# Kernel optimization log

Hardware: AMD Instinct MI355X
Metric: run time of the kernel (lower is better)

## Reference

```python
import jax, jax.numpy as jnp
import numpy as np

V, E, F, L, S, B, C = 30522, 768, 3072, 4, 512, 32, 2


def _layernorm(x, g, b, eps=1e-5):
    mu = jnp.mean(x, axis=-1, keepdims=True)
    var = jnp.var(x, axis=-1, keepdims=True)
    return (x - mu) * jax.lax.rsqrt(var + eps) * g + b


def setup_inputs() -> dict:
    key = jax.random.key(0)
    ks = jax.random.split(key, 24)
    s = 0.02
    inp = {
        "input_ids": jax.random.randint(ks[0], (S, B), 0, V),
        "tok_emb": jax.random.normal(ks[1], (V, E), jnp.float32) * s,
        "pos_emb": jax.random.normal(ks[2], (512, E), jnp.float32) * s,
        "Wq": jax.random.normal(ks[3], (L, E, E), jnp.float32) * s,
        "bq": jnp.zeros((L, E), jnp.float32),
        "Wk": jax.random.normal(ks[4], (L, E, E), jnp.float32) * s,
        "bk": jnp.zeros((L, E), jnp.float32),
        "Wv": jax.random.normal(ks[5], (L, E, E), jnp.float32) * s,
        "bv": jnp.zeros((L, E), jnp.float32),
        "Wo": jax.random.normal(ks[6], (L, E, E), jnp.float32) * s,
        "bo": jnp.zeros((L, E), jnp.float32),
        "g1": jnp.ones((L, E), jnp.float32),
        "beta1": jnp.zeros((L, E), jnp.float32),
        "g2": jnp.ones((L, E), jnp.float32),
        "beta2": jnp.zeros((L, E), jnp.float32),
        "W1": jax.random.normal(ks[7], (L, E, F), jnp.float32) * s,
        "bf1": jnp.zeros((L, F), jnp.float32),
        "W2": jax.random.normal(ks[8], (L, F, E), jnp.float32) * s,
        "bf2": jnp.zeros((L, E), jnp.float32),
        "Wc": jax.random.normal(ks[9], (E, C), jnp.float32) * s,
        "bc": jnp.zeros((C,), jnp.float32),
    }
    return inp


def reference(input_ids, tok_emb, pos_emb, Wq, bq, Wk, bk, Wv, bv, Wo, bo,
              g1, beta1, g2, beta2, W1, bf1, W2, bf2, Wc, bc):
    s_len = input_ids.shape[0]
    # x: [S, B, E] (seq-first, as in the original)
    x = tok_emb[input_ids] + pos_emb[jnp.arange(s_len)][:, None, :]
    scale = 1.0 / jnp.sqrt(jnp.asarray(E, x.dtype))
    for l in range(L):
        Q = x @ Wq[l] + bq[l]
        K = x @ Wk[l] + bk[l]
        Vv = x @ Wv[l] + bv[l]
        # NOTE: faithful to source bug: attention mixes over BATCH dim, scores [S,B,B]
        scores = jnp.einsum('sbe,sce->sbc', Q, K) * scale
        attn = jax.nn.softmax(scores, axis=-1)
        ao = jnp.einsum('sbc,sce->sbe', attn, Vv)
        ao = ao @ Wo[l] + bo[l]
        x = _layernorm(x + ao, g1[l], beta1[l])
        h = jax.nn.relu(x @ W1[l] + bf1[l]) @ W2[l] + bf2[l]
        x = _layernorm(x + h, g2[l], beta2[l])
    cls = x[0]                      # [B, E]
    return cls @ Wc + bc            # [B, C]
```

## Files before the change

### kernel.cpp

```cpp
#include <hip/hip_runtime.h>


#define E_DIM 768
#define F_DIM 3072
#define L_NUM 4
#define S_LEN 512
#define NTOK  (S_LEN * 32)
#define QKVN  (3 * E_DIM)

typedef float f32x4 __attribute__((ext_vector_type(4)));
typedef unsigned int u32x4 __attribute__((ext_vector_type(4)));
typedef unsigned short u16x4 __attribute__((ext_vector_type(4)));

__device__ __forceinline__ float bf2f(unsigned int bits) {
    return __uint_as_float(bits << 16);
}
__device__ __forceinline__ unsigned short f2bf(float f) {
    unsigned int x = __float_as_uint(f);
    return (unsigned short)((x + 0x7fffu + ((x >> 16) & 1u)) >> 16);
}

#define GLD16(gp, lp) \
    __builtin_amdgcn_global_load_lds( \
        (const __attribute__((address_space(1))) unsigned int*)(gp), \
        (__attribute__((address_space(3))) unsigned int*)(lp), 16, 0, 0)

__global__ __launch_bounds__(256)
void tr_k(const float* __restrict__ src, unsigned short* __restrict__ dst,
          int R, int C, size_t ss, size_t ds)
{
    __shared__ float tile[32][33];
    src += (size_t)blockIdx.z * ss;
    dst += (size_t)blockIdx.z * ds;
    const int r0 = blockIdx.y * 32, c0 = blockIdx.x * 32;
    const int tr = threadIdx.x >> 3, tc = (threadIdx.x & 7) * 4;
    f32x4 v = *(const f32x4*)(src + (size_t)(r0 + tr) * C + c0 + tc);
    tile[tr][tc + 0] = v[0]; tile[tr][tc + 1] = v[1];
    tile[tr][tc + 2] = v[2]; tile[tr][tc + 3] = v[3];
    __syncthreads();
    u16x4 o;
    o[0] = f2bf(tile[tc + 0][tr]); o[1] = f2bf(tile[tc + 1][tr]);
    o[2] = f2bf(tile[tc + 2][tr]); o[3] = f2bf(tile[tc + 3][tr]);
    *(u16x4*)(dst + (size_t)(c0 + tr) * R + r0 + tc) = o;
}

__global__ __launch_bounds__(256)
void biascat_k(const float* __restrict__ bq, const float* __restrict__ bk,
               const float* __restrict__ bv, float* __restrict__ bqkv)
{
    const int i = blockIdx.x * 256 + threadIdx.x;
    if (i >= L_NUM * QKVN) return;
    const int l = i / QKVN, n = i % QKVN;
    float v;
    if (n < 768)       v = bq[l * 768 + n];
    else if (n < 1536) v = bk[l * 768 + n - 768];
    else               v = bv[l * 768 + n - 1536];
    bqkv[i] = v;
}

__global__ __launch_bounds__(256)
void embed_k(const int* __restrict__ ids, const float* __restrict__ tok,
             const float* __restrict__ pos, float* __restrict__ xf,
             unsigned short* __restrict__ xb)
{
    const int row = blockIdx.x;
    const int s = row >> 5;
    const int id = ids[row];
    const size_t rb = (size_t)row * E_DIM;
    for (int e = threadIdx.x; e < E_DIM; e += 256) {
        float v = tok[(size_t)id * E_DIM + e] + pos[(size_t)s * E_DIM + e];
        xf[rb + e] = v;
        xb[rb + e] = f2bf(v);
    }
}

template<int MODE>
__global__ __launch_bounds__(256)
void gemm2_k(const unsigned short* __restrict__ A, const unsigned short* __restrict__ BT,
             const float* __restrict__ bias, void* __restrict__ Cout,
             int lda, int ldb, int ldc, int K, int JT)
{
    __shared__ unsigned short As[128 * 64];
    __shared__ unsigned short Bs[128 * 64];
    const int t = threadIdx.x;
    const int d = blockIdx.x;
    const int qd = d >> 3, rd = d & 7;
    const int jb = qd % JT;
    const int ib = rd + 8 * (qd / JT);
    const int i0 = ib * 128, j0 = jb * 128;

    const int lane = t & 63, wave = t >> 6;
    const int wm = wave >> 1, wn = wave & 1;
    const int lr = lane & 15, lg = lane >> 4;

    const int sr = t >> 3;
    const int sc = (t & 7) * 8;

    f32x4 acc[4][4];
    #pragma unroll
    for (int mf = 0; mf < 4; mf++)
        #pragma unroll
        for (int nf = 0; nf < 4; nf++) acc[mf][nf] = (f32x4)0.0f;

    const unsigned short* Ab = A  + (size_t)(i0 + sr) * lda + sc;
    const unsigned short* Bb = BT + (size_t)(j0 + sr) * ldb + sc;
    unsigned short* Asp = &As[sr * 64 + sc];
    unsigned short* Bsp = &Bs[sr * 64 + sc];

    for (int k0 = 0; k0 < K; k0 += 64) {
        __syncthreads();
        #pragma unroll
        for (int c = 0; c < 4; c++) {
            GLD16(Ab + (size_t)(32 * c) * lda + k0, Asp + 32 * c * 64);
            GLD16(Bb + (size_t)(32 * c) * ldb + k0, Bsp + 32 * c * 64);
        }
        asm volatile("s_waitcnt vmcnt(0)" ::: "memory");
        __syncthreads();
        #pragma unroll
        for (int kk = 0; kk < 64; kk += 32) {
            u32x4 a[4], b[4];
            #pragma unroll
            for (int f = 0; f < 4; f++) {
                a[f] = *(const u32x4*)(&As[(wm * 64 + f * 16 + lr) * 64 + kk + lg * 8]);
                b[f] = *(const u32x4*)(&Bs[(wn * 64 + f * 16 + lr) * 64 + kk + lg * 8]);
            }
            #pragma unroll
            for (int mf = 0; mf < 4; mf++)
                #pragma unroll
                for (int nf = 0; nf < 4; nf++)
                    asm volatile("v_mfma_f32_16x16x32_bf16 %0, %1, %2, %0"
                                 : "+v"(acc[mf][nf]) : "v"(a[mf]), "v"(b[nf]));
        }
    }
    asm volatile("s_nop 7\n\ts_nop 7");
    #pragma unroll
    for (int nf = 0; nf < 4; nf++) {
        const int col = j0 + wn * 64 + nf * 16 + lr;
        const float bv = bias ? bias[col] : 0.0f;
        #pragma unroll
        for (int mf = 0; mf < 4; mf++) {
            #pragma unroll
            for (int jj = 0; jj < 4; jj++) {
                const int row = i0 + wm * 64 + mf * 16 + lg * 4 + jj;
                const size_t idx = (size_t)row * ldc + col;
                float v = acc[mf][nf][jj] + bv;
                if (MODE == 1) v = fmaxf(v, 0.0f);
                if (MODE == 2) ((float*)Cout)[idx] += v;
                else           ((unsigned short*)Cout)[idx] = f2bf(v);
            }
        }
    }
}

__global__ __launch_bounds__(1024)
void attn_k(unsigned short* __restrict__ qkv)
{
    __shared__ unsigned short Ks[32 * 776];
    __shared__ float attn_s[32 * 33];
    __shared__ float attn_t[32 * 36];
    const int s = blockIdx.x;
    const int t = threadIdx.x;
    const int base = s * 32;

    for (int ch = t; ch < 32 * 96; ch += 1024) {
        const int r = ch / 96, e = (ch % 96) * 8;
        *(u32x4*)(&Ks[r * 776 + e]) =
            *(const u32x4*)(qkv + (size_t)(base + r) * QKVN + 768 + e);
    }
    __syncthreads();
    {
        const int q = t >> 5, c = t & 31;
        const unsigned short* Qg = qkv + (size_t)(base + q) * QKVN;
        float acc = 0.f;
        for (int e = 0; e < E_DIM; e += 8) {
            u32x4 qv = *(const u32x4*)(Qg + e);
            u32x4 kv = *(const u32x4*)(&Ks[c * 776 + e]);
            #pragma unroll
            for (int w = 0; w < 4; w++) {
                acc += bf2f(qv[w] & 0xffffu) * bf2f(kv[w] & 0xffffu);
                acc += bf2f(qv[w] >> 16)     * bf2f(kv[w] >> 16);
            }
        }
        attn_s[q * 33 + c] = acc * 0.036084391824351615f;
    }
    __syncthreads();
    if (t < 32) {
        float mx = -1e30f;
        #pragma unroll
        for (int c = 0; c < 32; c++) mx = fmaxf(mx, attn_s[t * 33 + c]);
        float sum = 0.f;
        #pragma unroll
        for (int c = 0; c < 32; c++) sum += expf(attn_s[t * 33 + c] - mx);
        const float r = 1.0f / sum;
        #pragma unroll
        for (int c = 0; c < 32; c++)
            attn_t[c * 36 + t] = expf(attn_s[t * 33 + c] - mx) * r;
    }
    __syncthreads();
    if (t < E_DIM) {
        float o[32];
        #pragma unroll
        for (int q = 0; q < 32; q++) o[q] = 0.f;
        for (int c = 0; c < 32; c++) {
            const float vv = bf2f(qkv[(size_t)(base + c) * QKVN + 1536 + t]);
            const f32x4* arow = (const f32x4*)(&attn_t[c * 36]);
            #pragma unroll
            for (int q8 = 0; q8 < 8; q8++) {
                f32x4 a4 = arow[q8];
                o[q8 * 4 + 0] += a4[0] * vv;
                o[q8 * 4 + 1] += a4[1] * vv;
                o[q8 * 4 + 2] += a4[2] * vv;
                o[q8 * 4 + 3] += a4[3] * vv;
            }
        }
        #pragma unroll
        for (int q = 0; q < 32; q++)
            qkv[(size_t)(base + q) * QKVN + t] = f2bf(o[q]);
    }
}

__global__ __launch_bounds__(256)
void ln_k(float* x, const float* __restrict__ g, const float* __restrict__ bta,
          unsigned short* __restrict__ xbo)
{
    __shared__ float red[8];
    const int row = blockIdx.x, t = threadIdx.x;
    const size_t rb = (size_t)row * E_DIM;
    float v[3];
    float s = 0.f, s2 = 0.f;
    #pragma unroll
    for (int i = 0; i < 3; i++) {
        const float a = x[rb + t + i * 256];
        v[i] = a; s += a; s2 += a * a;
    }
    #pragma unroll
    for (int o = 32; o > 0; o >>= 1) { s += __shfl_down(s, o); s2 += __shfl_down(s2, o); }
    const int wv_ = t >> 6;
    if ((t & 63) == 0) { red[wv_] = s; red[4 + wv_] = s2; }
    __syncthreads();
    if (t == 0) {
        red[0] = red[0] + red[1] + red[2] + red[3];
        red[4] = red[4] + red[5] + red[6] + red[7];
    }
    __syncthreads();
    const float mu   = red[0] * (1.f / E_DIM);
    const float var  = red[4] * (1.f / E_DIM) - mu * mu;
    const float rinv = rsqrtf(var + 1e-5f);
    #pragma unroll
    for (int i = 0; i < 3; i++) {
        const int e = t + i * 256;
        const float y = (v[i] - mu) * rinv * g[e] + bta[e];
        x[rb + e] = y;
        xbo[rb + e] = f2bf(y);
    }
}

__global__ __launch_bounds__(256)
void cls_k(const float* __restrict__ xf, const float* __restrict__ Wc,
           const float* __restrict__ bc, float* __restrict__ out)
{
    __shared__ float red[256];
    const int t = threadIdx.x;
    const int o = t >> 2, p = t & 3;
    const int b = o >> 1, c = o & 1;
    float acc = 0.f;
    for (int e = p; e < E_DIM; e += 4)
        acc += xf[(size_t)b * E_DIM + e] * Wc[e * 2 + c];
    red[t] = acc;
    __syncthreads();
    if (p == 0) out[o] = red[t] + red[t + 1] + red[t + 2] + red[t + 3] + bc[c];
}

extern "C" void kernel_launch(void* const* d_in, const int* in_sizes, int n_in,
                              void* d_out, int out_size, void* d_ws, size_t ws_size,
                              hipStream_t stream)
{
    (void)in_sizes; (void)n_in; (void)out_size; (void)ws_size;
    const int*   ids = (const int*)  d_in[0];
    const float* tok = (const float*)d_in[1];
    const float* pos = (const float*)d_in[2];
    const float* Wq  = (const float*)d_in[3];
    const float* bq  = (const float*)d_in[4];
    const float* Wk  = (const float*)d_in[5];
    const float* bk  = (const float*)d_in[6];
    const float* Wv  = (const float*)d_in[7];
    const float* bv  = (const float*)d_in[8];
    const float* Wo  = (const float*)d_in[9];
    const float* bo  = (const float*)d_in[10];
    const float* g1  = (const float*)d_in[11];
    const float* be1 = (const float*)d_in[12];
    const float* g2  = (const float*)d_in[13];
    const float* be2 = (const float*)d_in[14];
    const float* W1  = (const float*)d_in[15];
    const float* bf1 = (const float*)d_in[16];
    const float* W2  = (const float*)d_in[17];
    const float* bf2 = (const float*)d_in[18];
    const float* Wc  = (const float*)d_in[19];
    const float* bc  = (const float*)d_in[20];
    float* out = (float*)d_out;

    char* p = (char*)d_ws;
    auto carve = [&](size_t bytes) { char* r = p; p += (bytes + 255) & ~(size_t)255; return r; };
    const size_t NE = (size_t)NTOK * E_DIM;
    float*          xf    = (float*)carve(NE * 4);
    unsigned short* xb    = (unsigned short*)carve(NE * 2);
    unsigned short* qkv   = (unsigned short*)carve((size_t)NTOK * QKVN * 2);
    unsigned short* wqkvT = (unsigned short*)carve((size_t)L_NUM * QKVN * E_DIM * 2);
    unsigned short* woT   = (unsigned short*)carve((size_t)L_NUM * E_DIM * E_DIM * 2);
    unsigned short* w1T   = (unsigned short*)carve((size_t)L_NUM * F_DIM * E_DIM * 2);
    unsigned short* w2T   = (unsigned short*)carve((size_t)L_NUM * E_DIM * F_DIM * 2);
    float*          bqkv  = (float*)carve((size_t)L_NUM * QKVN * 4);
    unsigned short* h1c   = qkv;

    const size_t sEE = (size_t)E_DIM * E_DIM, sEF = (size_t)E_DIM * F_DIM;
    tr_k<<<dim3(24, 24, 4), 256, 0, stream>>>(Wq, wqkvT,              768, 768, sEE, (size_t)QKVN * E_DIM);
    tr_k<<<dim3(24, 24, 4), 256, 0, stream>>>(Wk, wqkvT + 768 * 768,  768, 768, sEE, (size_t)QKVN * E_DIM);
    tr_k<<<dim3(24, 24, 4), 256, 0, stream>>>(Wv, wqkvT + 1536 * 768, 768, 768, sEE, (size_t)QKVN * E_DIM);
    tr_k<<<dim3(24, 24, 4), 256, 0, stream>>>(Wo, woT, 768, 768, sEE, sEE);
    tr_k<<<dim3(96, 24, 4), 256, 0, stream>>>(W1, w1T, 768, 3072, sEF, sEF);
    tr_k<<<dim3(24, 96, 4), 256, 0, stream>>>(W2, w2T, 3072, 768, sEF, sEF);
    biascat_k<<<(L_NUM * QKVN + 255) / 256, 256, 0, stream>>>(bq, bk, bv, bqkv);

    embed_k<<<NTOK, 256, 0, stream>>>(ids, tok, pos, xf, xb);

    const int IT = NTOK / 128;
    for (int l = 0; l < L_NUM; l++) {
        const unsigned short* wqkv_l = wqkvT + (size_t)l * QKVN * E_DIM;
        const unsigned short* wo_l   = woT + (size_t)l * sEE;
        const unsigned short* w1_l   = w1T + (size_t)l * sEF;
        const unsigned short* w2_l   = w2T + (size_t)l * sEF;

        gemm2_k<0><<<IT * 18, 256, 0, stream>>>(xb, wqkv_l, bqkv + l * QKVN, qkv,
                                                E_DIM, E_DIM, QKVN, E_DIM, 18);
        attn_k<<<S_LEN, 1024, 0, stream>>>(qkv);
        gemm2_k<2><<<IT * 6, 256, 0, stream>>>(qkv, wo_l, bo + l * E_DIM, xf,
                                               QKVN, E_DIM, E_DIM, E_DIM, 6);
        ln_k<<<NTOK, 256, 0, stream>>>(xf, g1 + l * E_DIM, be1 + l * E_DIM, xb);
        for (int c = 0; c < 2; c++) {
            const int c0 = c * 1536;
            gemm2_k<1><<<IT * 12, 256, 0, stream>>>(xb, w1_l + (size_t)c0 * E_DIM,
                                                    bf1 + (size_t)l * F_DIM + c0, h1c,
                                                    E_DIM, E_DIM, 1536, E_DIM, 12);
            gemm2_k<2><<<IT * 6, 256, 0, stream>>>(h1c, w2_l + c0,
                                                   c == 0 ? (bf2 + l * E_DIM) : (const float*)nullptr,
                                                   xf, 1536, F_DIM, E_DIM, 1536, 6);
        }
        ln_k<<<NTOK, 256, 0, stream>>>(xf, g2 + l * E_DIM, be2 + l * E_DIM, xb);
    }

    cls_k<<<1, 256, 0, stream>>>(xf, Wc, bc, out);
}
```

Before: 2.103 ms.

## Use MFMA for batch-attention scores and run the FFN unchunked when workspace allows

The attention kernel now computes the 32x32 QK^T scores with one wavefront issuing bf16 MFMA instructions straight from global memory, and does the softmax with in-register shuffles. This removes the LDS staging of K, the scalar dot-product loop and the serial single-thread softmax, and drops the block to 768 threads. Separately, when the workspace is large enough for the full 3072-wide hidden activation, the FFN runs as one W1 GEMM and one W2 GEMM instead of two chunked passes. That avoids a second read-modify-write of xf and halves the FFN launches, at the cost of a larger scratch buffer.

```diff
diff --git a/kernel.cpp b/kernel.cpp
--- a/kernel.cpp
+++ b/kernel.cpp
@@ -152,49 +152,61 @@
     }
 }
 
-__global__ __launch_bounds__(1024)
+__global__ __launch_bounds__(768)
 void attn_k(unsigned short* __restrict__ qkv)
 {
-    __shared__ unsigned short Ks[32 * 776];
-    __shared__ float attn_s[32 * 33];
     __shared__ float attn_t[32 * 36];
     const int s = blockIdx.x;
     const int t = threadIdx.x;
     const int base = s * 32;
 
-    for (int ch = t; ch < 32 * 96; ch += 1024) {
-        const int r = ch / 96, e = (ch % 96) * 8;
-        *(u32x4*)(&Ks[r * 776 + e]) =
-            *(const u32x4*)(qkv + (size_t)(base + r) * QKVN + 768 + e);
-    }
-    __syncthreads();
-    {
-        const int q = t >> 5, c = t & 31;
-        const unsigned short* Qg = qkv + (size_t)(base + q) * QKVN;
-        float acc = 0.f;
-        for (int e = 0; e < E_DIM; e += 8) {
-            u32x4 qv = *(const u32x4*)(Qg + e);
-            u32x4 kv = *(const u32x4*)(&Ks[c * 776 + e]);
-            #pragma unroll
-            for (int w = 0; w < 4; w++) {
-                acc += bf2f(qv[w] & 0xffffu) * bf2f(kv[w] & 0xffffu);
-                acc += bf2f(qv[w] >> 16)     * bf2f(kv[w] >> 16);
-            }
-        }
-        attn_s[q * 33 + c] = acc * 0.036084391824351615f;
-    }
-    __syncthreads();
-    if (t < 32) {
-        float mx = -1e30f;
-        #pragma unroll
-        for (int c = 0; c < 32; c++) mx = fmaxf(mx, attn_s[t * 33 + c]);
-        float sum = 0.f;
-        #pragma unroll
-        for (int c = 0; c < 32; c++) sum += expf(attn_s[t * 33 + c] - mx);
-        const float r = 1.0f / sum;
-        #pragma unroll
-        for (int c = 0; c < 32; c++)
-            attn_t[c * 36 + t] = expf(attn_s[t * 33 + c] - mx) * r;
+    if (t < 64) {
+        const int lr = t & 15, lg = t >> 4;
+        f32x4 sacc[2][2];
+        #pragma unroll
+        for (int m = 0; m < 2; m++)
+            #pragma unroll
+            for (int n = 0; n < 2; n++) sacc[m][n] = (f32x4)0.0f;
+        const unsigned short* Qb = qkv + (size_t)base * QKVN;
+        #pragma unroll 4
+        for (int k0 = 0; k0 < E_DIM; k0 += 32) {
+            u32x4 a0 = *(const u32x4*)(Qb + (size_t)lr        * QKVN + k0 + lg * 8);
+            u32x4 a1 = *(const u32x4*)(Qb + (size_t)(16 + lr) * QKVN + k0 + lg * 8);
+            u32x4 b0 = *(const u32x4*)(Qb + (size_t)lr        * QKVN + 768 + k0 + lg * 8);
+            u32x4 b1 = *(const u32x4*)(Qb + (size_t)(16 + lr) * QKVN + 768 + k0 + lg * 8);
+            asm volatile("v_mfma_f32_16x16x32_bf16 %0, %1, %2, %0" : "+v"(sacc[0][0]) : "v"(a0), "v"(b0));
+            asm volatile("v_mfma_f32_16x16x32_bf16 %0, %1, %2, %0" : "+v"(sacc[0][1]) : "v"(a0), "v"(b1));
+            asm volatile("v_mfma_f32_16x16x32_bf16 %0, %1, %2, %0" : "+v"(sacc[1][0]) : "v"(a1), "v"(b0));
+            asm volatile("v_mfma_f32_16x16x32_bf16 %0, %1, %2, %0" : "+v"(sacc[1][1]) : "v"(a1), "v"(b1));
+        }
+        asm volatile("s_nop 7\n\ts_nop 7");
+        const float scale = 0.036084391824351615f;
+        float p[2][2][4];
+        #pragma unroll
+        for (int m = 0; m < 2; m++) {
+            #pragma unroll
+            for (int j = 0; j < 4; j++) {
+                float v0 = sacc[m][0][j] * scale;
+                float v1 = sacc[m][1][j] * scale;
+                float mx = fmaxf(v0, v1);
+                #pragma unroll
+                for (int o = 1; o < 16; o <<= 1) mx = fmaxf(mx, __shfl_xor(mx, o));
+                float e0 = expf(v0 - mx), e1 = expf(v1 - mx);
+                float sm = e0 + e1;
+                #pragma unroll
+                for (int o = 1; o < 16; o <<= 1) sm += __shfl_xor(sm, o);
+                const float r = 1.0f / sm;
+                p[m][0][j] = e0 * r;
+                p[m][1][j] = e1 * r;
+            }
+        }
+        #pragma unroll
+        for (int m = 0; m < 2; m++)
+            #pragma unroll
+            for (int n = 0; n < 2; n++)
+                #pragma unroll
+                for (int j = 0; j < 4; j++)
+                    attn_t[(n * 16 + lr) * 36 + m * 16 + lg * 4 + j] = p[m][n][j];
     }
     __syncthreads();
     if (t < E_DIM) {
@@ -275,7 +287,7 @@
                               void* d_out, int out_size, void* d_ws, size_t ws_size,
                               hipStream_t stream)
 {
-    (void)in_sizes; (void)n_in; (void)out_size; (void)ws_size;
+    (void)in_sizes; (void)n_in; (void)out_size;
     const int*   ids = (const int*)  d_in[0];
     const float* tok = (const float*)d_in[1];
     const float* pos = (const float*)d_in[2];
@@ -299,20 +311,28 @@
     const float* bc  = (const float*)d_in[20];
     float* out = (float*)d_out;
 
+    auto al = [](size_t b) { return (b + 255) & ~(size_t)255; };
+    const size_t NE = (size_t)NTOK * E_DIM;
+    const size_t sEE = (size_t)E_DIM * E_DIM, sEF = (size_t)E_DIM * F_DIM;
+    const size_t fixed = al(NE * 4) + al(NE * 2)
+                       + al((size_t)L_NUM * QKVN * E_DIM * 2) + al((size_t)L_NUM * sEE * 2)
+                       + al((size_t)L_NUM * sEF * 2) + al((size_t)L_NUM * sEF * 2)
+                       + al((size_t)L_NUM * QKVN * 4);
+    const bool big = ws_size >= fixed + al((size_t)NTOK * F_DIM * 2);
+
     char* p = (char*)d_ws;
     auto carve = [&](size_t bytes) { char* r = p; p += (bytes + 255) & ~(size_t)255; return r; };
-    const size_t NE = (size_t)NTOK * E_DIM;
     float*          xf    = (float*)carve(NE * 4);
     unsigned short* xb    = (unsigned short*)carve(NE * 2);
-    unsigned short* qkv   = (unsigned short*)carve((size_t)NTOK * QKVN * 2);
+    unsigned short* qkv   = (unsigned short*)carve(big ? (size_t)NTOK * F_DIM * 2
+                                                       : (size_t)NTOK * QKVN * 2);
     unsigned short* wqkvT = (unsigned short*)carve((size_t)L_NUM * QKVN * E_DIM * 2);
-    unsigned short* woT   = (unsigned short*)carve((size_t)L_NUM * E_DIM * E_DIM * 2);
-    unsigned short* w1T   = (unsigned short*)carve((size_t)L_NUM * F_DIM * E_DIM * 2);
-    unsigned short* w2T   = (unsigned short*)carve((size_t)L_NUM * E_DIM * F_DIM * 2);
+    unsigned short* woT   = (unsigned short*)carve((size_t)L_NUM * sEE * 2);
+    unsigned short* w1T   = (unsigned short*)carve((size_t)L_NUM * sEF * 2);
+    unsigned short* w2T   = (unsigned short*)carve((size_t)L_NUM * sEF * 2);
     float*          bqkv  = (float*)carve((size_t)L_NUM * QKVN * 4);
     unsigned short* h1c   = qkv;
 
-    const size_t sEE = (size_t)E_DIM * E_DIM, sEF = (size_t)E_DIM * F_DIM;
     tr_k<<<dim3(24, 24, 4), 256, 0, stream>>>(Wq, wqkvT,              768, 768, sEE, (size_t)QKVN * E_DIM);
     tr_k<<<dim3(24, 24, 4), 256, 0, stream>>>(Wk, wqkvT + 768 * 768,  768, 768, sEE, (size_t)QKVN * E_DIM);
     tr_k<<<dim3(24, 24, 4), 256, 0, stream>>>(Wv, wqkvT + 1536 * 768, 768, 768, sEE, (size_t)QKVN * E_DIM);
@@ -332,18 +352,25 @@
 
         gemm2_k<0><<<IT * 18, 256, 0, stream>>>(xb, wqkv_l, bqkv + l * QKVN, qkv,
                                                 E_DIM, E_DIM, QKVN, E_DIM, 18);
-        attn_k<<<S_LEN, 1024, 0, stream>>>(qkv);
+        attn_k<<<S_LEN, 768, 0, stream>>>(qkv);
         gemm2_k<2><<<IT * 6, 256, 0, stream>>>(qkv, wo_l, bo + l * E_DIM, xf,
                                                QKVN, E_DIM, E_DIM, E_DIM, 6);
         ln_k<<<NTOK, 256, 0, stream>>>(xf, g1 + l * E_DIM, be1 + l * E_DIM, xb);
-        for (int c = 0; c < 2; c++) {
-            const int c0 = c * 1536;
-            gemm2_k<1><<<IT * 12, 256, 0, stream>>>(xb, w1_l + (size_t)c0 * E_DIM,
-                                                    bf1 + (size_t)l * F_DIM + c0, h1c,
-                                                    E_DIM, E_DIM, 1536, E_DIM, 12);
-            gemm2_k<2><<<IT * 6, 256, 0, stream>>>(h1c, w2_l + c0,
-                                                   c == 0 ? (bf2 + l * E_DIM) : (const float*)nullptr,
-                                                   xf, 1536, F_DIM, E_DIM, 1536, 6);
+        if (big) {
+            gemm2_k<1><<<IT * 24, 256, 0, stream>>>(xb, w1_l, bf1 + (size_t)l * F_DIM, h1c,
+                                                    E_DIM, E_DIM, F_DIM, E_DIM, 24);
+            gemm2_k<2><<<IT * 6, 256, 0, stream>>>(h1c, w2_l, bf2 + l * E_DIM, xf,
+                                                   F_DIM, F_DIM, E_DIM, F_DIM, 6);
+        } else {
+            for (int c = 0; c < 2; c++) {
+                const int c0 = c * 1536;
+                gemm2_k<1><<<IT * 12, 256, 0, stream>>>(xb, w1_l + (size_t)c0 * E_DIM,
+                                                        bf1 + (size_t)l * F_DIM + c0, h1c,
+                                                        E_DIM, E_DIM, 1536, E_DIM, 12);
+                gemm2_k<2><<<IT * 6, 256, 0, stream>>>(h1c, w2_l + c0,
+                                                       c == 0 ? (bf2 + l * E_DIM) : (const float*)nullptr,
+                                                       xf, 1536, F_DIM, E_DIM, 1536, 6);
+            }
         }
         ln_k<<<NTOK, 256, 0, stream>>>(xf, g2 + l * E_DIM, be2 + l * E_DIM, xb);
     }
```

After: 1.870 ms. -11.1%, faster.
